# Optimization experiments

Measured on AMD Instinct MI355X. Metric: run time of the kernel, lower is better.

Reference implementation:

```python
import jax, jax.numpy as jnp
import numpy as np

B, D_IN, P, K = 65536, 1408, 256, 64
COMMIT = 0.25
LN_EPS = 1e-5
NORM_EPS = 1e-12  # torch F.normalize eps


def _l2norm(x):
    return x / jnp.maximum(jnp.linalg.norm(x, axis=-1, keepdims=True), NORM_EPS)


def setup_inputs() -> dict:
    key = jax.random.key(0)
    k0, k1, k2 = jax.random.split(key, 3)
    z_frame = jax.random.normal(k0, (B, D_IN), dtype=jnp.float32)
    # nn.Linear(input_dim, projection_dim)
    bound = 1.0 / np.sqrt(D_IN)
    W = jax.random.uniform(k1, (D_IN, P), minval=-bound, maxval=bound, dtype=jnp.float32)
    b = jnp.zeros((P,), jnp.float32)
    # nn.LayerNorm(projection_dim)
    gamma = jnp.ones((P,), jnp.float32)
    beta = jnp.zeros((P,), jnp.float32)
    # registered codebook buffer: normalized random rows
    codebook = _l2norm(jax.random.normal(k2, (K, P), dtype=jnp.float32))
    return {"z_frame": z_frame, "W": W, "b": b, "gamma": gamma, "beta": beta, "codebook": codebook}


def reference(z_frame, W, b, gamma, beta, codebook):
    # L2 normalize frame vectors
    z_norm = _l2norm(z_frame)                       # [B, D_in]
    # projection: Linear + LayerNorm
    h = z_norm @ W + b                              # [B, P]
    mu = jnp.mean(h, axis=-1, keepdims=True)
    var = jnp.mean(jnp.square(h - mu), axis=-1, keepdims=True)
    z_proj = (h - mu) / jnp.sqrt(var + LN_EPS) * gamma + beta
    z = _l2norm(z_proj)                             # [B, P]
    # squared euclidean distance to codebook
    dist = (jnp.sum(z * z, axis=1, keepdims=True)
            - 2.0 * (z @ codebook.T)
            + jnp.sum(codebook * codebook, axis=1))  # [B, K]
    indices = jnp.argmin(dist, axis=1)              # [B]
    z_q = codebook[indices]                         # [B, P]
    loss = COMMIT * jnp.mean(jnp.square(jax.lax.stop_gradient(z_q) - z))
    z_q_st = z + jax.lax.stop_gradient(z_q - z)     # straight-through
    return z_q_st, indices, loss
```

## Files before the change

kernel.cpp:

```cpp
#include <hip/hip_runtime.h>
#include <math.h>
#include <float.h>

#define NB    65536
#define DIN   1408
#define PDIM  256
#define KCB   64
#define TAU   3e-4f

#define OFF_CNT   0
#define OFF_CAND  64
#define OFF_LIST  262208
#define OFF_PART  524352
#define OFF_G     1048832

typedef short bf16x8 __attribute__((ext_vector_type(8)));
typedef float f32x4  __attribute__((ext_vector_type(4)));

static __device__ __forceinline__ float wave_sum(float v) {
#pragma unroll
  for (int m = 32; m; m >>= 1) v += __shfl_xor(v, m, 64);
  return v;
}

static __device__ __forceinline__ ushort4 split_hi(float4 v, float4& lo) {
  unsigned int ux = __float_as_uint(v.x), uy = __float_as_uint(v.y),
               uz = __float_as_uint(v.z), uw = __float_as_uint(v.w);
  lo.x = v.x - __uint_as_float(ux & 0xffff0000u);
  lo.y = v.y - __uint_as_float(uy & 0xffff0000u);
  lo.z = v.z - __uint_as_float(uz & 0xffff0000u);
  lo.w = v.w - __uint_as_float(uw & 0xffff0000u);
  return make_ushort4((unsigned short)(ux >> 16), (unsigned short)(uy >> 16),
                      (unsigned short)(uz >> 16), (unsigned short)(uw >> 16));
}
static __device__ __forceinline__ ushort4 rne4(float4 v) {
  return make_ushort4((unsigned short)((__float_as_uint(v.x) + 0x8000u) >> 16),
                      (unsigned short)((__float_as_uint(v.y) + 0x8000u) >> 16),
                      (unsigned short)((__float_as_uint(v.z) + 0x8000u) >> 16),
                      (unsigned short)((__float_as_uint(v.w) + 0x8000u) >> 16));
}

#define ROWS 40
__global__ __launch_bounds__(512, 2) void k2_gemm(const float* __restrict__ A,
                                                  const float* __restrict__ W,
                                                  float* __restrict__ g) {
  __shared__ unsigned short As_hi[128][ROWS], As_lo[128][ROWS];
  __shared__ unsigned short Ws_hi[PDIM][ROWS], Ws_lo[PDIM][ROWS];
  __shared__ float rn[128];
  const int t = threadIdx.x;
  const int lane = t & 63;
  const int wm = (t >> 6) >> 2, wn = (t >> 6) & 3;
  const int row0 = blockIdx.x * 128;
  const int ar = t >> 2, ak = (t & 3) << 3;
  const int wcol = t >> 1, wkg = (t & 1) << 4;
  const float* Ap = A + (size_t)(row0 + ar) * DIN + ak;
  const float* Wp = W + (size_t)wkg * PDIM + wcol;

  const f32x4 zero = {0.f, 0.f, 0.f, 0.f};
  f32x4 acc[4][4];
#pragma unroll
  for (int i = 0; i < 4; ++i)
#pragma unroll
    for (int j = 0; j < 4; ++j) acc[i][j] = zero;

  float4 a0 = *(const float4*)(Ap);
  float4 a1 = *(const float4*)(Ap + 4);
  float wv[16];
#pragma unroll
  for (int i = 0; i < 16; ++i) wv[i] = Wp[(size_t)i * PDIM];

  float ss = 0.f;
  for (int k0 = 0; k0 < DIN; k0 += 32) {
    ss += a0.x * a0.x + a0.y * a0.y + a0.z * a0.z + a0.w * a0.w
        + a1.x * a1.x + a1.y * a1.y + a1.z * a1.z + a1.w * a1.w;
    {
      float4 lo;
      ushort4 h = split_hi(a0, lo);
      *(ushort4*)&As_hi[ar][ak] = h;
      *(ushort4*)&As_lo[ar][ak] = rne4(lo);
      h = split_hi(a1, lo);
      *(ushort4*)&As_hi[ar][ak + 4] = h;
      *(ushort4*)&As_lo[ar][ak + 4] = rne4(lo);
#pragma unroll
      for (int q = 0; q < 4; ++q) {
        float4 wva = make_float4(wv[4 * q], wv[4 * q + 1], wv[4 * q + 2], wv[4 * q + 3]);
        float4 wlo;
        ushort4 wh = split_hi(wva, wlo);
        *(ushort4*)&Ws_hi[wcol][wkg + 4 * q] = wh;
        *(ushort4*)&Ws_lo[wcol][wkg + 4 * q] = rne4(wlo);
      }
    }
    __syncthreads();
    const int kn = (k0 + 32 < DIN) ? k0 + 32 : 0;
    float4 na0 = *(const float4*)(Ap + kn);
    float4 na1 = *(const float4*)(Ap + kn + 4);
    float nwv[16];
#pragma unroll
    for (int i = 0; i < 16; ++i) nwv[i] = Wp[(size_t)(kn + i) * PDIM];

    {
      const int fr = lane & 15, fq = (lane >> 4) << 3;
      bf16x8 ah[4], al[4], bh[4], bl[4];
#pragma unroll
      for (int mf = 0; mf < 4; ++mf) {
        const int r = (wm << 6) + (mf << 4) + fr;
        ah[mf] = *(const bf16x8*)&As_hi[r][fq];
        al[mf] = *(const bf16x8*)&As_lo[r][fq];
      }
#pragma unroll
      for (int nf = 0; nf < 4; ++nf) {
        const int n = (wn << 6) + (nf << 4) + fr;
        bh[nf] = *(const bf16x8*)&Ws_hi[n][fq];
        bl[nf] = *(const bf16x8*)&Ws_lo[n][fq];
      }
#pragma unroll
      for (int mf = 0; mf < 4; ++mf)
#pragma unroll
        for (int nf = 0; nf < 4; ++nf) {
          acc[mf][nf] = __builtin_amdgcn_mfma_f32_16x16x32_bf16(ah[mf], bh[nf], acc[mf][nf], 0, 0, 0);
          acc[mf][nf] = __builtin_amdgcn_mfma_f32_16x16x32_bf16(al[mf], bh[nf], acc[mf][nf], 0, 0, 0);
          acc[mf][nf] = __builtin_amdgcn_mfma_f32_16x16x32_bf16(ah[mf], bl[nf], acc[mf][nf], 0, 0, 0);
        }
    }
    __syncthreads();
    a0 = na0; a1 = na1;
#pragma unroll
    for (int i = 0; i < 16; ++i) wv[i] = nwv[i];
  }

  ss += __shfl_xor(ss, 1, 64);
  ss += __shfl_xor(ss, 2, 64);
  if ((t & 3) == 0) rn[ar] = ss;
  __syncthreads();
  if (t < 128) rn[t] = 1.0f / fmaxf(sqrtf(rn[t]), 1e-12f);
  __syncthreads();

  const int er = lane & 15, eq = (lane >> 4) << 2;
#pragma unroll
  for (int mf = 0; mf < 4; ++mf) {
#pragma unroll
    for (int nf = 0; nf < 4; ++nf) {
#pragma unroll
      for (int r = 0; r < 4; ++r) {
        const int row = (wm << 6) + (mf << 4) + eq + r;
        const int col = (wn << 6) + (nf << 4) + er;
        g[(size_t)(row0 + row) * PDIM + col] = acc[mf][nf][r] * rn[row];
      }
    }
  }
}

#define RB 64
#define CPAD 260
__global__ __launch_bounds__(256, 1) void k3_epilogue(const float* __restrict__ g,
                                                      const float* __restrict__ bvec,
                                                      const float* __restrict__ gamma,
                                                      const float* __restrict__ beta,
                                                      const float* __restrict__ C,
                                                      float* __restrict__ out,
                                                      int* __restrict__ cand,
                                                      int* __restrict__ list,
                                                      int* __restrict__ cnt,
                                                      double* __restrict__ partials) {
  __shared__ float Cs[KCB][CPAD];
  __shared__ float zsh[RB][CPAD];
  __shared__ float ccs[KCB];
  __shared__ float zzs[RB];
  __shared__ float lb[RB];
  __shared__ int idxsh[RB];
  const int t = threadIdx.x;
  const int lane = t & 63, w = t >> 6;
  const int row0 = blockIdx.x * RB;

  float4 creg[16];
#pragma unroll
  for (int i = 0; i < 16; ++i)
    creg[i] = *(const float4*)(C + (size_t)((t + (i << 8)) << 2));
#pragma unroll
  for (int i = 0; i < 16; ++i) {
    const int idx = t + (i << 8);
    *(float4*)&Cs[idx >> 6][(idx & 63) << 2] = creg[i];
  }
  __syncthreads();

  {
    const int kr = t >> 2, q = t & 3;
    float s = 0.f;
#pragma unroll
    for (int c = 0; c < 16; ++c) {
      float4 v = *(const float4*)&Cs[kr][(q << 6) + (c << 2)];
      s += v.x * v.x + v.y * v.y + v.z * v.z + v.w * v.w;
    }
    s += __shfl_xor(s, 1, 64);
    s += __shfl_xor(s, 2, 64);
    if (q == 0) ccs[kr] = s;
  }

  float4 bv = *(const float4*)(bvec + (lane << 2));
  float4 gm = *(const float4*)(gamma + (lane << 2));
  float4 bt = *(const float4*)(beta + (lane << 2));
  float4 gvv[16];
#pragma unroll
  for (int rr = 0; rr < 16; ++rr)
    gvv[rr] = *(const float4*)(g + (size_t)(row0 + (w << 4) + rr) * PDIM + (lane << 2));
#pragma unroll
  for (int rr = 0; rr < 16; ++rr) {
    const int r = (w << 4) + rr;
    float h0 = gvv[rr].x + bv.x, h1 = gvv[rr].y + bv.y;
    float h2 = gvv[rr].z + bv.z, h3 = gvv[rr].w + bv.w;
    float mu = wave_sum(h0 + h1 + h2 + h3) * (1.0f / 256.0f);
    float d0 = h0 - mu, d1 = h1 - mu, d2 = h2 - mu, d3 = h3 - mu;
    float var = wave_sum(d0 * d0 + d1 * d1 + d2 * d2 + d3 * d3) * (1.0f / 256.0f);
    float invs = 1.0f / sqrtf(var + 1e-5f);
    float zp0 = d0 * invs * gm.x + bt.x, zp1 = d1 * invs * gm.y + bt.y;
    float zp2 = d2 * invs * gm.z + bt.z, zp3 = d3 * invs * gm.w + bt.w;
    float nz = wave_sum(zp0 * zp0 + zp1 * zp1 + zp2 * zp2 + zp3 * zp3);
    float zn = 1.0f / fmaxf(sqrtf(nz), 1e-12f);
    float z0 = zp0 * zn, z1 = zp1 * zn, z2 = zp2 * zn, z3 = zp3 * zn;
    float zz = wave_sum(z0 * z0 + z1 * z1 + z2 * z2 + z3 * z3);
    float4 zf = {z0, z1, z2, z3};
    *(float4*)&zsh[r][lane << 2] = zf;
    if (lane == 0) zzs[r] = zz;
  }
  __syncthreads();

  const int kg = t & 15, rg = t >> 4;
  float p[4][4];
#pragma unroll
  for (int i = 0; i < 4; ++i)
#pragma unroll
    for (int j = 0; j < 4; ++j) p[i][j] = 0.f;

#pragma unroll 2
  for (int c4 = 0; c4 < 64; ++c4) {
    const int co = c4 << 2;
    float4 cv[4], zv[4];
#pragma unroll
    for (int ki = 0; ki < 4; ++ki) cv[ki] = *(const float4*)&Cs[kg + (ki << 4)][co];
#pragma unroll
    for (int ri = 0; ri < 4; ++ri) zv[ri] = *(const float4*)&zsh[rg + (ri << 4)][co];
#pragma unroll
    for (int ki = 0; ki < 4; ++ki)
#pragma unroll
      for (int ri = 0; ri < 4; ++ri) {
        p[ki][ri] = fmaf(cv[ki].x, zv[ri].x, p[ki][ri]);
        p[ki][ri] = fmaf(cv[ki].y, zv[ri].y, p[ki][ri]);
        p[ki][ri] = fmaf(cv[ki].z, zv[ri].z, p[ki][ri]);
        p[ki][ri] = fmaf(cv[ki].w, zv[ri].w, p[ki][ri]);
      }
  }

  float ccl[4];
#pragma unroll
  for (int ki = 0; ki < 4; ++ki) ccl[ki] = ccs[kg + (ki << 4)];

  float b1[4], b2[4];
  int i1[4];
#pragma unroll
  for (int ri = 0; ri < 4; ++ri) {
    const float zz = zzs[rg + (ri << 4)];
    b1[ri] = zz - 2.0f * p[0][ri] + ccl[0];
    i1[ri] = kg;
    b2[ri] = FLT_MAX;
#pragma unroll
    for (int ki = 1; ki < 4; ++ki) {
      const float d = zz - 2.0f * p[ki][ri] + ccl[ki];
      if (d < b1[ri]) { b2[ri] = b1[ri]; b1[ri] = d; i1[ri] = kg + (ki << 4); }
      else b2[ri] = fminf(b2[ri], d);
    }
  }
#pragma unroll
  for (int m = 1; m < 16; m <<= 1) {
#pragma unroll
    for (int ri = 0; ri < 4; ++ri) {
      float ob1 = __shfl_xor(b1[ri], m, 64);
      int oi1 = __shfl_xor(i1[ri], m, 64);
      float ob2 = __shfl_xor(b2[ri], m, 64);
      if (ob1 < b1[ri] || (ob1 == b1[ri] && oi1 < i1[ri])) {
        b2[ri] = fminf(b1[ri], ob2);
        b1[ri] = ob1; i1[ri] = oi1;
      } else {
        b2[ri] = fminf(b2[ri], ob1);
      }
    }
  }
  if (kg == 0) {
#pragma unroll
    for (int ri = 0; ri < 4; ++ri) {
      const int r = rg + (ri << 4);
      const int grow = row0 + r;
      cand[grow] = i1[ri];
      out[(size_t)NB * PDIM + grow] = (float)i1[ri];
      idxsh[r] = i1[ri];
      lb[r] = b1[ri];
      if (b2[ri] - b1[ri] < TAU) {
        int wpos = atomicAdd(cnt, 1);
        list[wpos] = grow;
      }
    }
  }
  __syncthreads();

#pragma unroll 4
  for (int rr = 0; rr < 16; ++rr) {
    const int r = (w << 4) + rr;
    const int ii = idxsh[r];
    float4 cv = *(const float4*)&Cs[ii][lane << 2];
    *(float4*)(out + (size_t)(row0 + r) * PDIM + (lane << 2)) = cv;
  }
  if (t == 0) {
    double s = 0.0;
    for (int r = 0; r < RB; ++r) s += (double)lb[r];
    partials[blockIdx.x] = s;
  }
}

__global__ __launch_bounds__(256) void k4_refine(const float* __restrict__ A,
                                                 const float* __restrict__ W,
                                                 const float* __restrict__ bvec,
                                                 const float* __restrict__ gamma,
                                                 const float* __restrict__ beta,
                                                 const float* __restrict__ C,
                                                 const int* __restrict__ list,
                                                 const int* __restrict__ cnt,
                                                 int* __restrict__ cand,
                                                 float* __restrict__ out,
                                                 double* __restrict__ partials) {
  __shared__ double xs[DIN];
  __shared__ double red[256];
  __shared__ double zd[PDIM];
  __shared__ int idx2[2];
  const int t = threadIdx.x;
  const int n = *cnt;
  for (int it = blockIdx.x; it < n; it += gridDim.x) {
    const int row = list[it];
    __syncthreads();
    for (int i = t; i < DIN; i += 256) xs[i] = (double)A[(size_t)row * DIN + i];
    __syncthreads();
    double s = 0.0;
    for (int i = t; i < DIN; i += 256) s += xs[i] * xs[i];
    red[t] = s; __syncthreads();
    for (int m = 128; m; m >>= 1) { if (t < m) red[t] += red[t + m]; __syncthreads(); }
    const double inv = 1.0 / fmax(sqrt(red[0]), 1e-12);

    double gj = 0.0;
#pragma unroll 8
    for (int k = 0; k < DIN; ++k) gj += xs[k] * (double)W[(size_t)k * PDIM + t];
    const double h = gj * inv + (double)bvec[t];

    __syncthreads(); red[t] = h; __syncthreads();
    for (int m = 128; m; m >>= 1) { if (t < m) red[t] += red[t + m]; __syncthreads(); }
    const double mu = red[0] * (1.0 / 256.0);
    const double d = h - mu;
    __syncthreads(); red[t] = d * d; __syncthreads();
    for (int m = 128; m; m >>= 1) { if (t < m) red[t] += red[t + m]; __syncthreads(); }
    const double invs = 1.0 / sqrt(red[0] * (1.0 / 256.0) + 1e-5);
    const double zp = d * invs * (double)gamma[t] + (double)beta[t];
    __syncthreads(); red[t] = zp * zp; __syncthreads();
    for (int m = 128; m; m >>= 1) { if (t < m) red[t] += red[t + m]; __syncthreads(); }
    const double zn = 1.0 / fmax(sqrt(red[0]), 1e-12);
    const double z = zp * zn;
    zd[t] = z;
    __syncthreads(); red[t] = z * z; __syncthreads();
    for (int m = 128; m; m >>= 1) { if (t < m) red[t] += red[t + m]; __syncthreads(); }
    const double zz = red[0];
    __syncthreads();
    if (t < KCB) {
      double p = 0.0, cc = 0.0;
      for (int c = 0; c < PDIM; ++c) {
        double cv = (double)C[(size_t)t * PDIM + c];
        p += zd[c] * cv; cc += cv * cv;
      }
      red[t] = zz - 2.0 * p + cc;
    }
    __syncthreads();
    if (t == 0) {
      double best = red[0]; int bi = 0;
      for (int k = 1; k < KCB; ++k) if (red[k] < best) { best = red[k]; bi = k; }
      const int old = cand[row];
      idx2[0] = bi; idx2[1] = old;
      if (bi != old) {
        cand[row] = bi;
        out[(size_t)NB * PDIM + row] = (float)bi;
        atomicAdd(&partials[row >> 6], red[bi] - red[old]);
      }
    }
    __syncthreads();
    if (idx2[0] != idx2[1])
      out[(size_t)row * PDIM + t] = C[(size_t)idx2[0] * PDIM + t];
    __syncthreads();
  }
}

__global__ __launch_bounds__(256) void k6_finalize(const double* __restrict__ partials,
                                                   float* __restrict__ out) {
  __shared__ double red[256];
  const int t = threadIdx.x;
  double s = 0.0;
  for (int i = t; i < NB / RB; i += 256) s += partials[i];
  red[t] = s; __syncthreads();
  for (int m = 128; m; m >>= 1) { if (t < m) red[t] += red[t + m]; __syncthreads(); }
  if (t == 0)
    out[(size_t)NB * PDIM + NB] = (float)(0.25 * red[0] / ((double)NB * (double)PDIM));
}

extern "C" void kernel_launch(void* const* d_in, const int* in_sizes, int n_in,
                              void* d_out, int out_size, void* d_ws, size_t ws_size,
                              hipStream_t stream) {
  const float* z_frame  = (const float*)d_in[0];
  const float* W        = (const float*)d_in[1];
  const float* bvec     = (const float*)d_in[2];
  const float* gamma    = (const float*)d_in[3];
  const float* beta     = (const float*)d_in[4];
  const float* codebook = (const float*)d_in[5];
  float* out = (float*)d_out;

  char* ws = (char*)d_ws;
  int*    cnt      = (int*)(ws + OFF_CNT);
  int*    cand     = (int*)(ws + OFF_CAND);
  int*    list     = (int*)(ws + OFF_LIST);
  double* partials = (double*)(ws + OFF_PART);
  float*  g        = (float*)(ws + OFF_G);

  hipMemsetAsync(ws + OFF_CNT, 0, 64, stream);

  k2_gemm<<<NB / 128, 512, 0, stream>>>(z_frame, W, g);
  k3_epilogue<<<NB / RB, 256, 0, stream>>>(g, bvec, gamma, beta, codebook,
                                           out, cand, list, cnt, partials);
  k4_refine<<<256, 256, 0, stream>>>(z_frame, W, bvec, gamma, beta, codebook,
                                     list, cnt, cand, out, partials);
  k6_finalize<<<1, 256, 0, stream>>>(partials, out);
}
```

Baseline: 917.3 us.

## Pre-split W into bf16 hi/lo tiles and stream them via global_load_lds

Adds a small pre-pass kernel that splits W once into hi/lo bf16 halves, laid out in swizzled 32-wide k-blocks. The GEMM then copies those halves straight into LDS with global_load_lds, so each block no longer repeats the strided fp32 W loads and the split on every tile. LDS rows shrink from padded 40 to 32 and use an XOR swizzle to avoid bank conflicts, and launch bounds now ask for more resident blocks. The converted weights sit temporarily in the output buffer, which depends on the later kernels overwriting that region.

```diff
diff --git a/kernel.cpp b/kernel.cpp
--- a/kernel.cpp
+++ b/kernel.cpp
@@ -7,14 +7,18 @@
 #define PDIM  256
 #define KCB   64
 #define TAU   3e-4f
+#define NKB   44
 
 #define OFF_CNT   0
 #define OFF_CAND  64
 #define OFF_LIST  262208
 #define OFF_PART  524352
 #define OFF_G     1048832
+#define WT_US     360448
+#define WTL_OFS   368640
 
 typedef short bf16x8 __attribute__((ext_vector_type(8)));
+typedef unsigned short us8 __attribute__((ext_vector_type(8)));
 typedef float f32x4  __attribute__((ext_vector_type(4)));
 
 static __device__ __forceinline__ float wave_sum(float v) {
@@ -23,38 +27,57 @@
   return v;
 }
 
-static __device__ __forceinline__ ushort4 split_hi(float4 v, float4& lo) {
-  unsigned int ux = __float_as_uint(v.x), uy = __float_as_uint(v.y),
-               uz = __float_as_uint(v.z), uw = __float_as_uint(v.w);
-  lo.x = v.x - __uint_as_float(ux & 0xffff0000u);
-  lo.y = v.y - __uint_as_float(uy & 0xffff0000u);
-  lo.z = v.z - __uint_as_float(uz & 0xffff0000u);
-  lo.w = v.w - __uint_as_float(uw & 0xffff0000u);
-  return make_ushort4((unsigned short)(ux >> 16), (unsigned short)(uy >> 16),
-                      (unsigned short)(uz >> 16), (unsigned short)(uw >> 16));
-}
-static __device__ __forceinline__ ushort4 rne4(float4 v) {
-  return make_ushort4((unsigned short)((__float_as_uint(v.x) + 0x8000u) >> 16),
-                      (unsigned short)((__float_as_uint(v.y) + 0x8000u) >> 16),
-                      (unsigned short)((__float_as_uint(v.z) + 0x8000u) >> 16),
-                      (unsigned short)((__float_as_uint(v.w) + 0x8000u) >> 16));
-}
-
-#define ROWS 40
-__global__ __launch_bounds__(512, 2) void k2_gemm(const float* __restrict__ A,
-                                                  const float* __restrict__ W,
+static __device__ __forceinline__ void gl_lds16(const void* gsrc, void* ldst) {
+  __builtin_amdgcn_global_load_lds(
+      (const __attribute__((address_space(1))) unsigned int*)gsrc,
+      (__attribute__((address_space(3))) unsigned int*)ldst, 16, 0, 0);
+}
+
+__global__ __launch_bounds__(256) void k1_wconv(const float* __restrict__ W,
+                                                unsigned short* __restrict__ WTh,
+                                                unsigned short* __restrict__ WTl) {
+  const int gg = blockIdx.x * 256 + threadIdx.x;
+  const int kb = gg >> 10;
+  const int rem = gg & 1023;
+  const int col = rem >> 2;
+  const int qp = rem & 3;
+  const int q = qp ^ ((col >> 1) & 3);
+  const int kbase = kb * 32 + q * 8;
+  us8 h8, l8;
+#pragma unroll
+  for (int j = 0; j < 8; ++j) {
+    float v = W[(size_t)(kbase + j) * PDIM + col];
+    unsigned u = __float_as_uint(v);
+    float hif = __uint_as_float(u & 0xffff0000u);
+    h8[j] = (unsigned short)(u >> 16);
+    l8[j] = (unsigned short)((__float_as_uint(v - hif) + 0x8000u) >> 16);
+  }
+  *(us8*)(WTh + ((size_t)gg << 3)) = h8;
+  *(us8*)(WTl + ((size_t)gg << 3)) = l8;
+}
+
+__global__ __launch_bounds__(512, 6) void k2_gemm(const float* __restrict__ A,
+                                                  const unsigned short* __restrict__ WTh,
+                                                  const unsigned short* __restrict__ WTl,
                                                   float* __restrict__ g) {
-  __shared__ unsigned short As_hi[128][ROWS], As_lo[128][ROWS];
-  __shared__ unsigned short Ws_hi[PDIM][ROWS], Ws_lo[PDIM][ROWS];
+  __shared__ unsigned short As_hi[128][32], As_lo[128][32];
+  __shared__ unsigned short Ws_hi[PDIM][32], Ws_lo[PDIM][32];
   __shared__ float rn[128];
   const int t = threadIdx.x;
   const int lane = t & 63;
-  const int wm = (t >> 6) >> 2, wn = (t >> 6) & 3;
+  const int w = t >> 6;
+  const int wm = w >> 2, wn = w & 3;
   const int row0 = blockIdx.x * 128;
-  const int ar = t >> 2, ak = (t & 3) << 3;
-  const int wcol = t >> 1, wkg = (t & 1) << 4;
-  const float* Ap = A + (size_t)(row0 + ar) * DIN + ak;
-  const float* Wp = W + (size_t)wkg * PDIM + wcol;
+  const int ar = t >> 2, aq = t & 3;
+  const int sa = (ar >> 1) & 3;
+  const int awoff = ar * 64 + ((aq ^ sa) << 4);
+  const float* Ap = A + (size_t)(row0 + ar) * DIN + (aq << 3);
+  const unsigned short* wsrc0 =
+      WTh + (size_t)((w << 4) + (lane >> 2)) * 32 + ((lane & 3) << 3);
+  const unsigned short* wsrc0l =
+      WTl + (size_t)((w << 4) + (lane >> 2)) * 32 + ((lane & 3) << 3);
+  char* wdstH = (char*)Ws_hi + (w << 10);
+  char* wdstL = (char*)Ws_lo + (w << 10);
 
   const f32x4 zero = {0.f, 0.f, 0.f, 0.f};
   f32x4 acc[4][4];
@@ -63,55 +86,56 @@
 #pragma unroll
     for (int j = 0; j < 4; ++j) acc[i][j] = zero;
 
+  const int fr = lane & 15, qd = lane >> 4;
+  const int qsw = ((qd ^ ((fr >> 1) & 3)) << 4);
+
   float4 a0 = *(const float4*)(Ap);
   float4 a1 = *(const float4*)(Ap + 4);
-  float wv[16];
-#pragma unroll
-  for (int i = 0; i < 16; ++i) wv[i] = Wp[(size_t)i * PDIM];
 
   float ss = 0.f;
-  for (int k0 = 0; k0 < DIN; k0 += 32) {
+  for (int kb = 0; kb < NKB; ++kb) {
+    {
+      const unsigned short* sh = wsrc0 + ((size_t)kb << 13);
+      const unsigned short* sl = wsrc0l + ((size_t)kb << 13);
+      gl_lds16(sh, wdstH);
+      gl_lds16(sh + 4096, wdstH + 8192);
+      gl_lds16(sl, wdstL);
+      gl_lds16(sl + 4096, wdstL + 8192);
+    }
     ss += a0.x * a0.x + a0.y * a0.y + a0.z * a0.z + a0.w * a0.w
         + a1.x * a1.x + a1.y * a1.y + a1.z * a1.z + a1.w * a1.w;
     {
-      float4 lo;
-      ushort4 h = split_hi(a0, lo);
-      *(ushort4*)&As_hi[ar][ak] = h;
-      *(ushort4*)&As_lo[ar][ak] = rne4(lo);
-      h = split_hi(a1, lo);
-      *(ushort4*)&As_hi[ar][ak + 4] = h;
-      *(ushort4*)&As_lo[ar][ak + 4] = rne4(lo);
-#pragma unroll
-      for (int q = 0; q < 4; ++q) {
-        float4 wva = make_float4(wv[4 * q], wv[4 * q + 1], wv[4 * q + 2], wv[4 * q + 3]);
-        float4 wlo;
-        ushort4 wh = split_hi(wva, wlo);
-        *(ushort4*)&Ws_hi[wcol][wkg + 4 * q] = wh;
-        *(ushort4*)&Ws_lo[wcol][wkg + 4 * q] = rne4(wlo);
-      }
-    }
-    __syncthreads();
-    const int kn = (k0 + 32 < DIN) ? k0 + 32 : 0;
+      us8 h8, l8;
+      float av[8] = {a0.x, a0.y, a0.z, a0.w, a1.x, a1.y, a1.z, a1.w};
+#pragma unroll
+      for (int j = 0; j < 8; ++j) {
+        unsigned u = __float_as_uint(av[j]);
+        float hif = __uint_as_float(u & 0xffff0000u);
+        h8[j] = (unsigned short)(u >> 16);
+        l8[j] = (unsigned short)((__float_as_uint(av[j] - hif) + 0x8000u) >> 16);
+      }
+      *(us8*)((char*)As_hi + awoff) = h8;
+      *(us8*)((char*)As_lo + awoff) = l8;
+    }
+    __syncthreads();
+
+    const int kn = (kb + 1 < NKB) ? (kb + 1) << 5 : 0;
     float4 na0 = *(const float4*)(Ap + kn);
     float4 na1 = *(const float4*)(Ap + kn + 4);
-    float nwv[16];
-#pragma unroll
-    for (int i = 0; i < 16; ++i) nwv[i] = Wp[(size_t)(kn + i) * PDIM];
 
     {
-      const int fr = lane & 15, fq = (lane >> 4) << 3;
       bf16x8 ah[4], al[4], bh[4], bl[4];
 #pragma unroll
       for (int mf = 0; mf < 4; ++mf) {
-        const int r = (wm << 6) + (mf << 4) + fr;
-        ah[mf] = *(const bf16x8*)&As_hi[r][fq];
-        al[mf] = *(const bf16x8*)&As_lo[r][fq];
+        const int off = ((wm << 6) + (mf << 4) + fr) * 64 + qsw;
+        ah[mf] = *(const bf16x8*)((const char*)As_hi + off);
+        al[mf] = *(const bf16x8*)((const char*)As_lo + off);
       }
 #pragma unroll
       for (int nf = 0; nf < 4; ++nf) {
-        const int n = (wn << 6) + (nf << 4) + fr;
-        bh[nf] = *(const bf16x8*)&Ws_hi[n][fq];
-        bl[nf] = *(const bf16x8*)&Ws_lo[n][fq];
+        const int off = ((wn << 6) + (nf << 4) + fr) * 64 + qsw;
+        bh[nf] = *(const bf16x8*)((const char*)Ws_hi + off);
+        bl[nf] = *(const bf16x8*)((const char*)Ws_lo + off);
       }
 #pragma unroll
       for (int mf = 0; mf < 4; ++mf)
@@ -124,8 +148,6 @@
     }
     __syncthreads();
     a0 = na0; a1 = na1;
-#pragma unroll
-    for (int i = 0; i < 16; ++i) wv[i] = nwv[i];
   }
 
   ss += __shfl_xor(ss, 1, 64);
@@ -422,9 +444,13 @@
   double* partials = (double*)(ws + OFF_PART);
   float*  g        = (float*)(ws + OFF_G);
 
+  unsigned short* WTh = (unsigned short*)out;
+  unsigned short* WTl = WTh + WTL_OFS;
+
   hipMemsetAsync(ws + OFF_CNT, 0, 64, stream);
 
-  k2_gemm<<<NB / 128, 512, 0, stream>>>(z_frame, W, g);
+  k1_wconv<<<176, 256, 0, stream>>>(W, WTh, WTl);
+  k2_gemm<<<NB / 128, 512, 0, stream>>>(z_frame, WTh, WTl, g);
   k3_epilogue<<<NB / RB, 256, 0, stream>>>(g, bvec, gamma, beta, codebook,
                                            out, cand, list, cnt, partials);
   k4_refine<<<256, 256, 0, stream>>>(z_frame, W, bvec, gamma, beta, codebook,
```

Result: slower. 2.152 ms (+134.6%).
